# Performance work log

Measured on AMD Instinct MI355X. Metric: run time of the kernel, lower is better.

## Reference

```python
import jax, jax.numpy as jnp
import numpy as np

B, S, D, H, DFF = 2, 4096, 768, 12, 3072
DH = D // H
EPS = 1e-6


def layer_norm(x, gamma, beta):
    # torch.std is unbiased (ddof=1); normalizer is (sigma + eps), NOT sqrt(var+eps)
    mu = jnp.mean(x, axis=-1, keepdims=True)
    sigma = jnp.sqrt(jnp.var(x, axis=-1, keepdims=True, ddof=1))
    return gamma * (x - mu) / (sigma + EPS) + beta


def setup_inputs() -> dict:
    key = jax.random.key(0)
    ks = jax.random.split(key, 12)
    sc = 1.0 / np.sqrt(D)
    inp = {
        "x": jax.random.normal(ks[0], (B, S, D), dtype=jnp.float32),
        "mask": jnp.ones((B, S, S), dtype=jnp.float32),  # multiplicative mask
        "wq": jax.random.normal(ks[1], (D, D), dtype=jnp.float32) * sc,
        "bq": jnp.zeros((D,), dtype=jnp.float32),
        "wk": jax.random.normal(ks[2], (D, D), dtype=jnp.float32) * sc,
        "bk": jnp.zeros((D,), dtype=jnp.float32),
        "wv": jax.random.normal(ks[3], (D, D), dtype=jnp.float32) * sc,
        "bv": jnp.zeros((D,), dtype=jnp.float32),
        "wo": jax.random.normal(ks[4], (D, D), dtype=jnp.float32) * sc,
        "bo": jnp.zeros((D,), dtype=jnp.float32),
        "w1": jax.random.normal(ks[5], (D, DFF), dtype=jnp.float32) * sc,
        "b1": jnp.zeros((DFF,), dtype=jnp.float32),
        "w2": jax.random.normal(ks[6], (DFF, D), dtype=jnp.float32) * (1.0 / np.sqrt(DFF)),
        "b2": jnp.zeros((D,), dtype=jnp.float32),
        "gamma1": jnp.ones((D,), dtype=jnp.float32),
        "beta1": jnp.zeros((D,), dtype=jnp.float32),
        "gamma2": jnp.ones((D,), dtype=jnp.float32),
        "beta2": jnp.zeros((D,), dtype=jnp.float32),
    }
    return inp


def reference(x, mask, wq, bq, wk, bk, wv, bv, wo, bo, w1, b1, w2, b2,
              gamma1, beta1, gamma2, beta2):
    # Pre-LN encoder layer (is_pre_layer_norm=True); dropout is identity (eval).
    l1 = layer_norm(x, gamma1, beta1)                      # [B,S,D]

    # --- multi-head self-attention ---
    q = (l1 @ wq + bq).reshape(B, S, H, DH).transpose(0, 2, 1, 3)  # [B,H,S,DH]
    k = (l1 @ wk + bk).reshape(B, S, H, DH).transpose(0, 2, 1, 3)
    v = (l1 @ wv + bv).reshape(B, S, H, DH).transpose(0, 2, 1, 3)
    scores = jnp.einsum("bhqd,bhkd->bhqk", q, k) / jnp.sqrt(jnp.float32(DH))
    scores = scores * mask[:, None, :, :]                  # multiplicative mask, pre-softmax
    attn = jax.nn.softmax(scores, axis=-1)                 # [B,H,S,S]
    ctx = jnp.einsum("bhqk,bhkd->bhqd", attn, v)           # [B,H,S,DH]
    ctx = ctx.transpose(0, 2, 1, 3).reshape(B, S, D)       # [B,S,D]
    a = ctx  # NOTE: original forward never applies out_linear in attention()... it does in forward
    a = ctx
    # MultiHeadAttention.forward returns the merged heads WITHOUT out_linear applied?
    # Re-check: forward() reshapes and returns `output` without out_linear in given code.
    x1 = x + a                                             # residual

    l2 = layer_norm(x1, gamma2, beta2)
    h = jax.nn.relu(l2 @ w1 + b1) @ w2 + b2                # FFN
    return h + x1
```

## Files before the change

### kernel.cpp

```cpp
#include <hip/hip_runtime.h>
#include <cstdint>
#include <cstddef>

#define BB   2
#define SEQ  4096
#define DD   768
#define HH   12
#define DHH  64
#define DFFN 3072
#define NTOK (BB*SEQ)

using bf16x8 = __attribute__((ext_vector_type(8))) __bf16;
using f32x4  = __attribute__((ext_vector_type(4))) float;
typedef unsigned int u32;

#define QK_SCALE 0.18033688011112042f

__device__ __forceinline__ float fast_exp2(float x) {
    return __builtin_amdgcn_exp2f(x);
}

__device__ __forceinline__ unsigned short f2bf(float f) {
    unsigned u = __float_as_uint(f);
    u = u + 0x7FFFu + ((u >> 16) & 1u);
    return (unsigned short)(u >> 16);
}
__device__ __forceinline__ unsigned short f2bf_trunc(float f) {
    return (unsigned short)(__float_as_uint(f) >> 16);
}

__device__ __forceinline__ bf16x8 ld_bf8(const unsigned short* p) {
    return *(const bf16x8*)p;
}

__device__ __forceinline__ void gl_lds16(const unsigned short* g, unsigned short* l) {
    __builtin_amdgcn_global_load_lds(
        (const __attribute__((address_space(1))) u32*)(uintptr_t)(const void*)g,
        (__attribute__((address_space(3))) u32*)(uintptr_t)(void*)l,
        16, 0, 0);
}

template <int N>
__device__ __forceinline__ float dpp_ror(float x) {
    return __int_as_float(__builtin_amdgcn_update_dpp(
        0, __float_as_int(x), 0x120 | N, 0xf, 0xf, false));
}
__device__ __forceinline__ float rowmax16(float x) {
    x = fmaxf(x, dpp_ror<1>(x));
    x = fmaxf(x, dpp_ror<2>(x));
    x = fmaxf(x, dpp_ror<4>(x));
    x = fmaxf(x, dpp_ror<8>(x));
    return x;
}
__device__ __forceinline__ float rowsum16(float x) {
    x += dpp_ror<1>(x);
    x += dpp_ror<2>(x);
    x += dpp_ror<4>(x);
    x += dpp_ror<8>(x);
    return x;
}

__global__ __launch_bounds__(256) void transpose_f32_to_bf16(
    const float* __restrict__ src, unsigned short* __restrict__ dst, int R, int C, float scale)
{
    __shared__ float tile[32][33];
    const int c0 = blockIdx.x * 32, r0 = blockIdx.y * 32;
    const int tx = threadIdx.x, ty = threadIdx.y;
#pragma unroll
    for (int i = 0; i < 32; i += 8)
        tile[ty + i][tx] = src[(size_t)(r0 + ty + i) * C + c0 + tx];
    __syncthreads();
#pragma unroll
    for (int i = 0; i < 32; i += 8)
        dst[(size_t)(c0 + ty + i) * R + r0 + tx] = f2bf(scale * tile[tx][ty + i]);
}

__global__ void concat_bias(const float* __restrict__ bq, const float* __restrict__ bk,
                            const float* __restrict__ bv, float* __restrict__ bqkv)
{
    int i = blockIdx.x * 256 + threadIdx.x;
    if (i < 3 * DD)
        bqkv[i] = (i < DD) ? bq[i] * QK_SCALE : (i < 2 * DD ? bk[i - DD] : bv[i - 2 * DD]);
}

__global__ __launch_bounds__(256) void mask_check(const float* __restrict__ mask, int* __restrict__ flag)
{
    const size_t n = (size_t)BB * SEQ * SEQ;
    const size_t stride = (size_t)gridDim.x * 1024;
    int bad = 0;
    for (size_t i = ((size_t)blockIdx.x * 256 + threadIdx.x) * 4; i < n; i += stride) {
        float4 v = *(const float4*)&mask[i];
        bad |= (v.x != 1.f) | (v.y != 1.f) | (v.z != 1.f) | (v.w != 1.f);
    }
    if (bad) atomicOr(flag, 1);
}

__global__ __launch_bounds__(256) void ln_fused(
    const float* __restrict__ x, const float* __restrict__ add,
    const float* __restrict__ gamma, const float* __restrict__ beta,
    unsigned short* __restrict__ out_ln, float* __restrict__ x1out)
{
    const int row = blockIdx.x, t = threadIdx.x;
    const size_t base = (size_t)row * DD;
    float v[3], s = 0.f, sq = 0.f;
#pragma unroll
    for (int p = 0; p < 3; ++p) {
        int idx = t + p * 256;
        float val = x[base + idx];
        if (add) val += add[base + idx];
        v[p] = val; s += val; sq += val * val;
    }
#pragma unroll
    for (int off = 1; off < 64; off <<= 1) {
        s  += __shfl_xor(s,  off);
        sq += __shfl_xor(sq, off);
    }
    __shared__ float red[8];
    const int wave = t >> 6;
    if ((t & 63) == 0) { red[wave] = s; red[4 + wave] = sq; }
    __syncthreads();
    s  = red[0] + red[1] + red[2] + red[3];
    sq = red[4] + red[5] + red[6] + red[7];
    const float mu   = s * (1.f / 768.f);
    const float var  = fmaxf((sq - 768.f * mu * mu) * (1.f / 767.f), 0.f);
    const float rstd = 1.f / (sqrtf(var) + 1e-6f);
#pragma unroll
    for (int p = 0; p < 3; ++p) {
        int idx = t + p * 256;
        if (x1out) x1out[base + idx] = v[p];
        out_ln[base + idx] = f2bf(gamma[idx] * (v[p] - mu) * rstd + beta[idx]);
    }
}

__global__ __launch_bounds__(256) void gemm_bf16(
    const unsigned short* __restrict__ A, const unsigned short* __restrict__ Bt,
    const float* __restrict__ bias, const float* __restrict__ resid,
    unsigned short* __restrict__ outB, float* __restrict__ outF,
    int M, int N, int K, int relu)
{
    __shared__ __align__(16) unsigned short As[128][64];
    __shared__ __align__(16) unsigned short Bs[128][64];
    const int tid = threadIdx.x;
    const int lane = tid & 63, wave = tid >> 6;
    const int quad = lane >> 4, l16 = lane & 15;
    const int wm = wave >> 1, wn = wave & 1;
    const int m0 = blockIdx.y * 128, n0 = blockIdx.x * 128;

    const f32x4 fzero = {0.f, 0.f, 0.f, 0.f};
    f32x4 acc[4][4];
#pragma unroll
    for (int i = 0; i < 4; ++i)
#pragma unroll
        for (int j = 0; j < 4; ++j) acc[i][j] = fzero;

    const int r  = tid >> 3;
    const int cg = tid & 7;

    for (int k0 = 0; k0 < K; k0 += 64) {
#pragma unroll
        for (int rr = 0; rr < 4; ++rr) {
            const int row = r + rr * 32;
            const int gc8 = (cg ^ (row & 7)) * 8;
            gl_lds16(&A [(size_t)(m0 + row) * K + k0 + gc8], &As[row][cg * 8]);
            gl_lds16(&Bt[(size_t)(n0 + row) * K + k0 + gc8], &Bs[row][cg * 8]);
        }
        __syncthreads();
#pragma unroll
        for (int ks = 0; ks < 2; ++ks) {
            bf16x8 af[4], bfv[4];
#pragma unroll
            for (int i = 0; i < 4; ++i) {
                const int row = wm * 64 + i * 16 + l16;
                af[i] = ld_bf8(&As[row][((ks * 4 + quad) ^ (row & 7)) * 8]);
            }
#pragma unroll
            for (int j = 0; j < 4; ++j) {
                const int row = wn * 64 + j * 16 + l16;
                bfv[j] = ld_bf8(&Bs[row][((ks * 4 + quad) ^ (row & 7)) * 8]);
            }
#pragma unroll
            for (int i = 0; i < 4; ++i)
#pragma unroll
                for (int j = 0; j < 4; ++j)
                    acc[i][j] = __builtin_amdgcn_mfma_f32_16x16x32_bf16(af[i], bfv[j], acc[i][j], 0, 0, 0);
        }
        __syncthreads();
    }
#pragma unroll
    for (int i = 0; i < 4; ++i)
#pragma unroll
        for (int j = 0; j < 4; ++j)
#pragma unroll
            for (int rr = 0; rr < 4; ++rr) {
                const int gm = m0 + wm * 64 + i * 16 + quad * 4 + rr;
                const int gn = n0 + wn * 64 + j * 16 + l16;
                float v = acc[i][j][rr] + bias[gn];
                if (relu) v = fmaxf(v, 0.f);
                if (resid) v += resid[(size_t)gm * N + gn];
                if (outF) outF[(size_t)gm * N + gn] = v;
                if (outB) outB[(size_t)gm * N + gn] = f2bf(v);
            }
}

__global__ __launch_bounds__(256) void vt_extract(
    const unsigned short* __restrict__ qkv, unsigned short* __restrict__ vtg)
{
    __shared__ unsigned short tile[64][72];
    const int bh = blockIdx.x, b = bh / HH, h = bh % HH;
    const int s0 = blockIdx.y * 64;
    const int tid = threadIdx.x;
#pragma unroll
    for (int p = 0; p < 2; ++p) {
        int idx = tid + p * 256;
        int r = idx >> 3, ch8 = (idx & 7) * 8;
        *(uint4*)&tile[r][ch8] =
            *(const uint4*)&qkv[(size_t)(b * SEQ + s0 + r) * 2304 + 1536 + h * 64 + ch8];
    }
    __syncthreads();
#pragma unroll
    for (int p = 0; p < 2; ++p) {
        int idx = tid + p * 256;
        int d = idx >> 3, sc = (idx & 7) * 8;
        unsigned short tmp[8];
#pragma unroll
        for (int j = 0; j < 8; ++j) tmp[j] = tile[sc + j][d];
        *(uint4*)&vtg[((size_t)bh * 64 + d) * SEQ + s0 + sc] = *(uint4*)tmp;
    }
}

__global__ __launch_bounds__(256, 2) void flash_attn5(
    const unsigned short* __restrict__ qkv, const unsigned short* __restrict__ vtg,
    const float* __restrict__ mask, const int* __restrict__ maskflag,
    float* __restrict__ ctx)
{
    __shared__ __align__(16) unsigned short Ks[128][72];
    __shared__ __align__(16) unsigned short Vt[64][136];
    __shared__ __align__(16) unsigned short Ps[4][2][16][136];
    const int tid = threadIdx.x;
    const int lane = tid & 63, wave = tid >> 6;
    const int quad = lane >> 4, l16 = lane & 15;
    const int bh = blockIdx.y, b = bh / HH, h = bh % HH;
    const int qbase = blockIdx.x * 128 + wave * 32;
    const int use_mask = *maskflag;

    bf16x8 qf[2][2];
#pragma unroll
    for (int mt = 0; mt < 2; ++mt) {
        const size_t qrow = (size_t)(b * SEQ + qbase + mt * 16 + l16) * 2304 + h * 64;
        qf[mt][0] = ld_bf8(&qkv[qrow + quad * 8]);
        qf[mt][1] = ld_bf8(&qkv[qrow + 32 + quad * 8]);
    }
    const f32x4 fzero = {0.f, 0.f, 0.f, 0.f};
    float l_run[2][4];
    f32x4 o[2][4];
#pragma unroll
    for (int mt = 0; mt < 2; ++mt)
#pragma unroll
        for (int r = 0; r < 4; ++r) { l_run[mt][r] = 0.f; o[mt][r] = fzero; }

    const float* mbase = mask + (size_t)b * SEQ * SEQ;
    const unsigned short* kgbase = qkv + (size_t)b * SEQ * 2304 + 768 + h * 64;
    const unsigned short* vgbase = vtg + (size_t)bh * 64 * SEQ;

    if (!use_mask) {
        float lsum[2][4];
#pragma unroll
        for (int mt = 0; mt < 2; ++mt)
#pragma unroll
            for (int r = 0; r < 4; ++r) lsum[mt][r] = 0.f;

        for (int k0 = 0; k0 < SEQ; k0 += 128) {
            __syncthreads();
#pragma unroll
            for (int p = 0; p < 4; ++p) {
                int idx = tid + p * 256;
                int row = idx >> 3, ch8 = (idx & 7) * 8;
                *(uint4*)&Ks[row][ch8] = *(const uint4*)&kgbase[(size_t)(k0 + row) * 2304 + ch8];
            }
#pragma unroll
            for (int p = 0; p < 4; ++p) {
                int idx = tid + p * 256;
                int d = idx >> 4, ch8 = (idx & 15) * 8;
                *(uint4*)&Vt[d][ch8] = *(const uint4*)&vgbase[(size_t)d * SEQ + k0 + ch8];
            }
            __syncthreads();

            f32x4 st[2][8];
#pragma unroll
            for (int j = 0; j < 8; ++j) {
                bf16x8 kf0 = ld_bf8(&Ks[j * 16 + l16][quad * 8]);
                bf16x8 kf1 = ld_bf8(&Ks[j * 16 + l16][32 + quad * 8]);
                st[0][j] = __builtin_amdgcn_mfma_f32_16x16x32_bf16(qf[0][0], kf0, fzero, 0, 0, 0);
                st[0][j] = __builtin_amdgcn_mfma_f32_16x16x32_bf16(qf[0][1], kf1, st[0][j], 0, 0, 0);
                st[1][j] = __builtin_amdgcn_mfma_f32_16x16x32_bf16(qf[1][0], kf0, fzero, 0, 0, 0);
                st[1][j] = __builtin_amdgcn_mfma_f32_16x16x32_bf16(qf[1][1], kf1, st[1][j], 0, 0, 0);
            }
#pragma unroll
            for (int mt = 0; mt < 2; ++mt) {
#pragma unroll
                for (int r = 0; r < 4; ++r) {
                    float acc = 0.f;
#pragma unroll
                    for (int j = 0; j < 8; ++j) {
                        float p = fast_exp2(st[mt][j][r]);
                        st[mt][j][r] = p;
                        acc += p;
                    }
                    lsum[mt][r] += acc;
                }
#pragma unroll
                for (int j = 0; j < 8; ++j)
#pragma unroll
                    for (int r = 0; r < 4; ++r)
                        Ps[wave][mt][quad * 4 + r][j * 16 + l16] = f2bf_trunc(st[mt][j][r]);
            }
#pragma unroll
            for (int kk = 0; kk < 4; ++kk) {
                bf16x8 pf0 = ld_bf8(&Ps[wave][0][l16][kk * 32 + quad * 8]);
                bf16x8 pf1 = ld_bf8(&Ps[wave][1][l16][kk * 32 + quad * 8]);
#pragma unroll
                for (int t = 0; t < 4; ++t) {
                    bf16x8 vf = ld_bf8(&Vt[t * 16 + l16][kk * 32 + quad * 8]);
                    o[0][t] = __builtin_amdgcn_mfma_f32_16x16x32_bf16(pf0, vf, o[0][t], 0, 0, 0);
                    o[1][t] = __builtin_amdgcn_mfma_f32_16x16x32_bf16(pf1, vf, o[1][t], 0, 0, 0);
                }
            }
        }
#pragma unroll
        for (int mt = 0; mt < 2; ++mt)
#pragma unroll
            for (int r = 0; r < 4; ++r) l_run[mt][r] = rowsum16(lsum[mt][r]);
    } else {
        float m_run[2][4];
#pragma unroll
        for (int mt = 0; mt < 2; ++mt)
#pragma unroll
            for (int r = 0; r < 4; ++r) m_run[mt][r] = -1e30f;

        for (int k0 = 0; k0 < SEQ; k0 += 128) {
            __syncthreads();
#pragma unroll
            for (int p = 0; p < 4; ++p) {
                int idx = tid + p * 256;
                int row = idx >> 3, ch8 = (idx & 7) * 8;
                *(uint4*)&Ks[row][ch8] = *(const uint4*)&kgbase[(size_t)(k0 + row) * 2304 + ch8];
            }
#pragma unroll
            for (int p = 0; p < 4; ++p) {
                int idx = tid + p * 256;
                int d = idx >> 4, ch8 = (idx & 15) * 8;
                *(uint4*)&Vt[d][ch8] = *(const uint4*)&vgbase[(size_t)d * SEQ + k0 + ch8];
            }
            __syncthreads();

            f32x4 st[2][8];
#pragma unroll
            for (int j = 0; j < 8; ++j) {
                bf16x8 kf0 = ld_bf8(&Ks[j * 16 + l16][quad * 8]);
                bf16x8 kf1 = ld_bf8(&Ks[j * 16 + l16][32 + quad * 8]);
                st[0][j] = __builtin_amdgcn_mfma_f32_16x16x32_bf16(qf[0][0], kf0, fzero, 0, 0, 0);
                st[0][j] = __builtin_amdgcn_mfma_f32_16x16x32_bf16(qf[0][1], kf1, st[0][j], 0, 0, 0);
                st[1][j] = __builtin_amdgcn_mfma_f32_16x16x32_bf16(qf[1][0], kf0, fzero, 0, 0, 0);
                st[1][j] = __builtin_amdgcn_mfma_f32_16x16x32_bf16(qf[1][1], kf1, st[1][j], 0, 0, 0);
            }
#pragma unroll
            for (int mt = 0; mt < 2; ++mt) {
                const int qr = qbase + mt * 16 + quad * 4;
#pragma unroll
                for (int r = 0; r < 4; ++r) {
                    const float* mrow = &mbase[(size_t)(qr + r) * SEQ + k0 + l16];
#pragma unroll
                    for (int j = 0; j < 8; ++j)
                        st[mt][j][r] *= mrow[j * 16];
                }
            }
#pragma unroll
            for (int mt = 0; mt < 2; ++mt) {
                float alpha[4];
#pragma unroll
                for (int r = 0; r < 4; ++r) {
                    float mx = st[mt][0][r];
#pragma unroll
                    for (int j = 1; j < 8; ++j) mx = fmaxf(mx, st[mt][j][r]);
                    mx = rowmax16(mx);
                    const float mnew = fmaxf(m_run[mt][r], mx);
                    alpha[r] = fast_exp2(m_run[mt][r] - mnew);
                    float ssum = 0.f;
#pragma unroll
                    for (int j = 0; j < 8; ++j) {
                        st[mt][j][r] = fast_exp2(st[mt][j][r] - mnew);
                        ssum += st[mt][j][r];
                    }
                    ssum = rowsum16(ssum);
                    l_run[mt][r] = l_run[mt][r] * alpha[r] + ssum;
                    m_run[mt][r] = mnew;
                }
#pragma unroll
                for (int t = 0; t < 4; ++t)
#pragma unroll
                    for (int r = 0; r < 4; ++r) o[mt][t][r] *= alpha[r];
#pragma unroll
                for (int j = 0; j < 8; ++j)
#pragma unroll
                    for (int r = 0; r < 4; ++r)
                        Ps[wave][mt][quad * 4 + r][j * 16 + l16] = f2bf_trunc(st[mt][j][r]);
            }
#pragma unroll
            for (int kk = 0; kk < 4; ++kk) {
                bf16x8 pf0 = ld_bf8(&Ps[wave][0][l16][kk * 32 + quad * 8]);
                bf16x8 pf1 = ld_bf8(&Ps[wave][1][l16][kk * 32 + quad * 8]);
#pragma unroll
                for (int t = 0; t < 4; ++t) {
                    bf16x8 vf = ld_bf8(&Vt[t * 16 + l16][kk * 32 + quad * 8]);
                    o[0][t] = __builtin_amdgcn_mfma_f32_16x16x32_bf16(pf0, vf, o[0][t], 0, 0, 0);
                    o[1][t] = __builtin_amdgcn_mfma_f32_16x16x32_bf16(pf1, vf, o[1][t], 0, 0, 0);
                }
            }
        }
    }

#pragma unroll
    for (int mt = 0; mt < 2; ++mt)
#pragma unroll
        for (int t = 0; t < 4; ++t)
#pragma unroll
            for (int r = 0; r < 4; ++r) {
                const int row = qbase + mt * 16 + quad * 4 + r;
                ctx[(size_t)(b * SEQ + row) * DD + h * 64 + t * 16 + l16] =
                    o[mt][t][r] / l_run[mt][r];
            }
}

extern "C" void kernel_launch(void* const* d_in, const int* in_sizes, int n_in,
                              void* d_out, int out_size, void* d_ws, size_t ws_size,
                              hipStream_t stream)
{
    (void)in_sizes; (void)n_in; (void)out_size; (void)ws_size;
    const float* x      = (const float*)d_in[0];
    const float* mask   = (const float*)d_in[1];
    const float* wq     = (const float*)d_in[2];
    const float* bq     = (const float*)d_in[3];
    const float* wk     = (const float*)d_in[4];
    const float* bk     = (const float*)d_in[5];
    const float* wv     = (const float*)d_in[6];
    const float* bv     = (const float*)d_in[7];
    const float* w1     = (const float*)d_in[10];
    const float* b1     = (const float*)d_in[11];
    const float* w2     = (const float*)d_in[12];
    const float* b2     = (const float*)d_in[13];
    const float* gamma1 = (const float*)d_in[14];
    const float* beta1  = (const float*)d_in[15];
    const float* gamma2 = (const float*)d_in[16];
    const float* beta2  = (const float*)d_in[17];
    float* out = (float*)d_out;

    char* ws = (char*)d_ws;
    size_t off = 0;
    auto take = [&](size_t bytes) -> char* {
        char* p = ws + off;
        off = (off + bytes + 255) & ~(size_t)255;
        return p;
    };
    unsigned short* wqkvT = (unsigned short*)take((size_t)2304 * 768 * 2);
    unsigned short* w1T   = (unsigned short*)take((size_t)3072 * 768 * 2);
    unsigned short* w2T   = (unsigned short*)take((size_t)768 * 3072 * 2);
    float*          bqkv  = (float*)take(2304 * 4);
    int*            mflag = (int*)take(256);
    unsigned short* l12   = (unsigned short*)take((size_t)NTOK * DD * 2);
    unsigned short* qkv   = (unsigned short*)take((size_t)NTOK * 2304 * 2);
    float*          x1    = (float*)take((size_t)NTOK * DD * 4);
    char*           big   = take((size_t)NTOK * DFFN * 2);
    float*          ctx   = (float*)big;
    unsigned short* vtg   = (unsigned short*)(big + (size_t)NTOK * DD * 4);
    unsigned short* hb    = (unsigned short*)big;

    (void)hipMemsetAsync(mflag, 0, 4, stream);
    mask_check<<<2048, 256, 0, stream>>>(mask, mflag);

    transpose_f32_to_bf16<<<dim3(24, 24), dim3(32, 8), 0, stream>>>(wq, wqkvT,                 768, 768, QK_SCALE);
    transpose_f32_to_bf16<<<dim3(24, 24), dim3(32, 8), 0, stream>>>(wk, wqkvT + 768 * 768,     768, 768, 1.0f);
    transpose_f32_to_bf16<<<dim3(24, 24), dim3(32, 8), 0, stream>>>(wv, wqkvT + 2 * 768 * 768, 768, 768, 1.0f);
    transpose_f32_to_bf16<<<dim3(96, 24), dim3(32, 8), 0, stream>>>(w1, w1T,                   768, 3072, 1.0f);
    transpose_f32_to_bf16<<<dim3(24, 96), dim3(32, 8), 0, stream>>>(w2, w2T,                   3072, 768, 1.0f);
    concat_bias<<<9, 256, 0, stream>>>(bq, bk, bv, bqkv);

    ln_fused<<<NTOK, 256, 0, stream>>>(x, nullptr, gamma1, beta1, l12, nullptr);
    gemm_bf16<<<dim3(2304 / 128, NTOK / 128), 256, 0, stream>>>(
        l12, wqkvT, bqkv, nullptr, qkv, nullptr, NTOK, 2304, 768, 0);
    vt_extract<<<dim3(BB * HH, SEQ / 64), 256, 0, stream>>>(qkv, vtg);
    flash_attn5<<<dim3(SEQ / 128, BB * HH), 256, 0, stream>>>(qkv, vtg, mask, mflag, ctx);
    ln_fused<<<NTOK, 256, 0, stream>>>(x, ctx, gamma2, beta2, l12, x1);
    gemm_bf16<<<dim3(3072 / 128, NTOK / 128), 256, 0, stream>>>(
        l12, w1T, b1, nullptr, hb, nullptr, NTOK, 3072, 768, 1);
    gemm_bf16<<<dim3(768 / 128, NTOK / 128), 256, 0, stream>>>(
        hb, w2T, b2, x1, nullptr, out, NTOK, 768, 3072, 0);
}
```

Before: 670.4 us.

## Double-buffer GEMM K-tiles and shrink attention P buffer for higher occupancy

The GEMM now stages 32-wide K slices into two LDS buffers, loading the next tile while MFMAs run on the current one. This drops one barrier per iteration and raises the occupancy hint to 3 blocks per CU. The attention kernel keeps only one 16-row P tile per wave by doing the PV product inside the per-mt loop, which cuts LDS use so its launch bound can also go to 3. It also replaces the per-element division in the output with a reciprocal multiply. Halving the K step doubles loop iterations, and the tighter occupancy hints may cause register spills.

New measurement: 678.0 us. About the same (+1.1%).

```diff
diff --git a/kernel.cpp b/kernel.cpp
--- a/kernel.cpp
+++ b/kernel.cpp
@@ -132,14 +132,14 @@
     }
 }
 
-__global__ __launch_bounds__(256) void gemm_bf16(
+__global__ __launch_bounds__(256, 3) void gemm_bf16(
     const unsigned short* __restrict__ A, const unsigned short* __restrict__ Bt,
     const float* __restrict__ bias, const float* __restrict__ resid,
     unsigned short* __restrict__ outB, float* __restrict__ outF,
     int M, int N, int K, int relu)
 {
-    __shared__ __align__(16) unsigned short As[128][64];
-    __shared__ __align__(16) unsigned short Bs[128][64];
+    __shared__ __align__(16) unsigned short As[2][128][32];
+    __shared__ __align__(16) unsigned short Bs[2][128][32];
     const int tid = threadIdx.x;
     const int lane = tid & 63, wave = tid >> 6;
     const int quad = lane >> 4, l16 = lane & 15;
@@ -153,38 +153,34 @@
 #pragma unroll
         for (int j = 0; j < 4; ++j) acc[i][j] = fzero;
 
-    const int r  = tid >> 3;
-    const int cg = tid & 7;
-
-    for (int k0 = 0; k0 < K; k0 += 64) {
-#pragma unroll
-        for (int rr = 0; rr < 4; ++rr) {
-            const int row = r + rr * 32;
-            const int gc8 = (cg ^ (row & 7)) * 8;
-            gl_lds16(&A [(size_t)(m0 + row) * K + k0 + gc8], &As[row][cg * 8]);
-            gl_lds16(&Bt[(size_t)(n0 + row) * K + k0 + gc8], &Bs[row][cg * 8]);
-        }
+    const int r2 = tid >> 2;
+    const int cg = tid & 3;
+    const int g0 = (cg ^ (r2 & 3)) * 8;
+
+    auto stage = [&](int buf, int k0) {
+        gl_lds16(&A [(size_t)(m0 + r2) * K + k0 + g0],       &As[buf][r2][cg * 8]);
+        gl_lds16(&A [(size_t)(m0 + 64 + r2) * K + k0 + g0],  &As[buf][64 + r2][cg * 8]);
+        gl_lds16(&Bt[(size_t)(n0 + r2) * K + k0 + g0],       &Bs[buf][r2][cg * 8]);
+        gl_lds16(&Bt[(size_t)(n0 + 64 + r2) * K + k0 + g0],  &Bs[buf][64 + r2][cg * 8]);
+    };
+
+    const int gsw = (quad ^ (l16 & 3)) * 8;
+    const int iters = K >> 5;
+    stage(0, 0);
+    for (int it = 0; it < iters; ++it) {
         __syncthreads();
-#pragma unroll
-        for (int ks = 0; ks < 2; ++ks) {
-            bf16x8 af[4], bfv[4];
-#pragma unroll
-            for (int i = 0; i < 4; ++i) {
-                const int row = wm * 64 + i * 16 + l16;
-                af[i] = ld_bf8(&As[row][((ks * 4 + quad) ^ (row & 7)) * 8]);
-            }
-#pragma unroll
-            for (int j = 0; j < 4; ++j) {
-                const int row = wn * 64 + j * 16 + l16;
-                bfv[j] = ld_bf8(&Bs[row][((ks * 4 + quad) ^ (row & 7)) * 8]);
-            }
-#pragma unroll
-            for (int i = 0; i < 4; ++i)
-#pragma unroll
-                for (int j = 0; j < 4; ++j)
-                    acc[i][j] = __builtin_amdgcn_mfma_f32_16x16x32_bf16(af[i], bfv[j], acc[i][j], 0, 0, 0);
-        }
-        __syncthreads();
+        if (it + 1 < iters) stage((it + 1) & 1, (it + 1) * 32);
+        const int buf = it & 1;
+        bf16x8 af[4], bfv[4];
+#pragma unroll
+        for (int i = 0; i < 4; ++i) af[i]  = ld_bf8(&As[buf][wm * 64 + i * 16 + l16][gsw]);
+#pragma unroll
+        for (int j = 0; j < 4; ++j) bfv[j] = ld_bf8(&Bs[buf][wn * 64 + j * 16 + l16][gsw]);
+#pragma unroll
+        for (int i = 0; i < 4; ++i)
+#pragma unroll
+            for (int j = 0; j < 4; ++j)
+                acc[i][j] = __builtin_amdgcn_mfma_f32_16x16x32_bf16(af[i], bfv[j], acc[i][j], 0, 0, 0);
     }
 #pragma unroll
     for (int i = 0; i < 4; ++i)
@@ -228,14 +224,14 @@
     }
 }
 
-__global__ __launch_bounds__(256, 2) void flash_attn5(
+__global__ __launch_bounds__(256, 3) void flash_attn6(
     const unsigned short* __restrict__ qkv, const unsigned short* __restrict__ vtg,
     const float* __restrict__ mask, const int* __restrict__ maskflag,
     float* __restrict__ ctx)
 {
     __shared__ __align__(16) unsigned short Ks[128][72];
     __shared__ __align__(16) unsigned short Vt[64][136];
-    __shared__ __align__(16) unsigned short Ps[4][2][16][136];
+    __shared__ __align__(16) unsigned short Ps[4][16][136];
     const int tid = threadIdx.x;
     const int lane = tid & 63, wave = tid >> 6;
     const int quad = lane >> 4, l16 = lane & 15;
@@ -312,17 +308,15 @@
                 for (int j = 0; j < 8; ++j)
 #pragma unroll
                     for (int r = 0; r < 4; ++r)
-                        Ps[wave][mt][quad * 4 + r][j * 16 + l16] = f2bf_trunc(st[mt][j][r]);
-            }
-#pragma unroll
-            for (int kk = 0; kk < 4; ++kk) {
-                bf16x8 pf0 = ld_bf8(&Ps[wave][0][l16][kk * 32 + quad * 8]);
-                bf16x8 pf1 = ld_bf8(&Ps[wave][1][l16][kk * 32 + quad * 8]);
-#pragma unroll
-                for (int t = 0; t < 4; ++t) {
-                    bf16x8 vf = ld_bf8(&Vt[t * 16 + l16][kk * 32 + quad * 8]);
-                    o[0][t] = __builtin_amdgcn_mfma_f32_16x16x32_bf16(pf0, vf, o[0][t], 0, 0, 0);
-                    o[1][t] = __builtin_amdgcn_mfma_f32_16x16x32_bf16(pf1, vf, o[1][t], 0, 0, 0);
+                        Ps[wave][quad * 4 + r][j * 16 + l16] = f2bf_trunc(st[mt][j][r]);
+#pragma unroll
+                for (int kk = 0; kk < 4; ++kk) {
+                    bf16x8 pf = ld_bf8(&Ps[wave][l16][kk * 32 + quad * 8]);
+#pragma unroll
+                    for (int t = 0; t < 4; ++t) {
+                        bf16x8 vf = ld_bf8(&Vt[t * 16 + l16][kk * 32 + quad * 8]);
+                        o[mt][t] = __builtin_amdgcn_mfma_f32_16x16x32_bf16(pf, vf, o[mt][t], 0, 0, 0);
+                    }
                 }
             }
         }
@@ -373,9 +367,6 @@
                     for (int j = 0; j < 8; ++j)
                         st[mt][j][r] *= mrow[j * 16];
                 }
-            }
-#pragma unroll
-            for (int mt = 0; mt < 2; ++mt) {
                 float alpha[4];
 #pragma unroll
                 for (int r = 0; r < 4; ++r) {
@@ -403,17 +394,15 @@
                 for (int j = 0; j < 8; ++j)
 #pragma unroll
                     for (int r = 0; r < 4; ++r)
-                        Ps[wave][mt][quad * 4 + r][j * 16 + l16] = f2bf_trunc(st[mt][j][r]);
-            }
-#pragma unroll
-            for (int kk = 0; kk < 4; ++kk) {
-                bf16x8 pf0 = ld_bf8(&Ps[wave][0][l16][kk * 32 + quad * 8]);
-                bf16x8 pf1 = ld_bf8(&Ps[wave][1][l16][kk * 32 + quad * 8]);
-#pragma unroll
-                for (int t = 0; t < 4; ++t) {
-                    bf16x8 vf = ld_bf8(&Vt[t * 16 + l16][kk * 32 + quad * 8]);
-                    o[0][t] = __builtin_amdgcn_mfma_f32_16x16x32_bf16(pf0, vf, o[0][t], 0, 0, 0);
-                    o[1][t] = __builtin_amdgcn_mfma_f32_16x16x32_bf16(pf1, vf, o[1][t], 0, 0, 0);
+                        Ps[wave][quad * 4 + r][j * 16 + l16] = f2bf_trunc(st[mt][j][r]);
+#pragma unroll
+                for (int kk = 0; kk < 4; ++kk) {
+                    bf16x8 pf = ld_bf8(&Ps[wave][l16][kk * 32 + quad * 8]);
+#pragma unroll
+                    for (int t = 0; t < 4; ++t) {
+                        bf16x8 vf = ld_bf8(&Vt[t * 16 + l16][kk * 32 + quad * 8]);
+                        o[mt][t] = __builtin_amdgcn_mfma_f32_16x16x32_bf16(pf, vf, o[mt][t], 0, 0, 0);
+                    }
                 }
             }
         }
@@ -422,13 +411,13 @@
 #pragma unroll
     for (int mt = 0; mt < 2; ++mt)
 #pragma unroll
-        for (int t = 0; t < 4; ++t)
-#pragma unroll
-            for (int r = 0; r < 4; ++r) {
-                const int row = qbase + mt * 16 + quad * 4 + r;
-                ctx[(size_t)(b * SEQ + row) * DD + h * 64 + t * 16 + l16] =
-                    o[mt][t][r] / l_run[mt][r];
-            }
+        for (int r = 0; r < 4; ++r) {
+            const float inv = 1.f / l_run[mt][r];
+            const int row = qbase + mt * 16 + quad * 4 + r;
+#pragma unroll
+            for (int t = 0; t < 4; ++t)
+                ctx[(size_t)(b * SEQ + row) * DD + h * 64 + t * 16 + l16] = o[mt][t][r] * inv;
+        }
 }
 
 extern "C" void kernel_launch(void* const* d_in, const int* in_sizes, int n_in,
@@ -488,7 +477,7 @@
     gemm_bf16<<<dim3(2304 / 128, NTOK / 128), 256, 0, stream>>>(
         l12, wqkvT, bqkv, nullptr, qkv, nullptr, NTOK, 2304, 768, 0);
     vt_extract<<<dim3(BB * HH, SEQ / 64), 256, 0, stream>>>(qkv, vtg);
-    flash_attn5<<<dim3(SEQ / 128, BB * HH), 256, 0, stream>>>(qkv, vtg, mask, mflag, ctx);
+    flash_attn6<<<dim3(SEQ / 128, BB * HH), 256, 0, stream>>>(qkv, vtg, mask, mflag, ctx);
     ln_fused<<<NTOK, 256, 0, stream>>>(x, ctx, gamma2, beta2, l12, x1);
     gemm_bf16<<<dim3(3072 / 128, NTOK / 128), 256, 0, stream>>>(
         l12, w1T, b1, nullptr, hb, nullptr, NTOK, 3072, 768, 1);
```
